# Performance work log

Hardware: AMD Instinct MI355X
Metric: run time of the kernel (lower is better)

Reference implementation:

```python
import jax, jax.numpy as jnp
import numpy as np

B, S, E, H, I = 32, 257, 1024, 16, 4096
D = E // H  # head_dim = 64
EPS = 1e-5


def setup_inputs() -> dict:
    key = jax.random.key(0)
    ks = jax.random.split(key, 12)
    std = 0.02
    inp = {
        'hidden_states': jax.random.normal(ks[0], (B, S, E), jnp.float32),
        'attention_mask': jnp.zeros((B, 1, S, S), jnp.float32),
        'causal_attention_mask': jnp.zeros((B, 1, S, S), jnp.float32),
        'ln1_w': jnp.ones((E,), jnp.float32),
        'ln1_b': jnp.zeros((E,), jnp.float32),
        'q_w': jax.random.normal(ks[1], (E, E), jnp.float32) * std,
        'q_b': jnp.zeros((E,), jnp.float32),
        'k_w': jax.random.normal(ks[2], (E, E), jnp.float32) * std,
        'k_b': jnp.zeros((E,), jnp.float32),
        'v_w': jax.random.normal(ks[3], (E, E), jnp.float32) * std,
        'v_b': jnp.zeros((E,), jnp.float32),
        'o_w': jax.random.normal(ks[4], (E, E), jnp.float32) * std,
        'o_b': jnp.zeros((E,), jnp.float32),
        'ln2_w': jnp.ones((E,), jnp.float32),
        'ln2_b': jnp.zeros((E,), jnp.float32),
        'fc1_w': jax.random.normal(ks[5], (I, E), jnp.float32) * std,
        'fc1_b': jnp.zeros((I,), jnp.float32),
        'fc2_w': jax.random.normal(ks[6], (E, I), jnp.float32) * std,
        'fc2_b': jnp.zeros((E,), jnp.float32),
    }
    return inp


def _layernorm(x, w, b):
    mu = jnp.mean(x, axis=-1, keepdims=True)
    var = jnp.mean(jnp.square(x - mu), axis=-1, keepdims=True)
    return (x - mu) * jax.lax.rsqrt(var + EPS) * w + b


def _gelu_tanh(x):
    # 0.5*x*(1+tanh(sqrt(2/pi)*(x+0.044715*x^3)))
    c = np.sqrt(2.0 / np.pi).astype(np.float32)
    return 0.5 * x * (1.0 + jnp.tanh(c * (x + 0.044715 * x * x * x)))


def reference(hidden_states, attention_mask, causal_attention_mask,
              ln1_w, ln1_b, q_w, q_b, k_w, k_b, v_w, v_b, o_w, o_b,
              ln2_w, ln2_b, fc1_w, fc1_b, fc2_w, fc2_b):
    scale = D ** -0.5
    residual = hidden_states
    x = _layernorm(hidden_states, ln1_w, ln1_b)

    # projections (torch Linear: x @ W.T + b), q pre-scaled as in source
    q = (x @ q_w.T + q_b) * scale
    k = x @ k_w.T + k_b
    v = x @ v_w.T + v_b

    # [B, H, S, D]
    q = q.reshape(B, S, H, D).transpose(0, 2, 1, 3)
    k = k.reshape(B, S, H, D).transpose(0, 2, 1, 3)
    v = v.reshape(B, S, H, D).transpose(0, 2, 1, 3)

    scores = jnp.einsum('bhqd,bhkd->bhqk', q, k)  # [B,H,S,S]
    scores = scores + causal_attention_mask + attention_mask
    probs = jax.nn.softmax(scores, axis=-1)
    ctx = jnp.einsum('bhqk,bhkd->bhqd', probs, v)
    ctx = ctx.transpose(0, 2, 1, 3).reshape(B, S, E)
    attn_out = ctx @ o_w.T + o_b

    h = residual + attn_out
    residual = h
    x = _layernorm(h, ln2_w, ln2_b)
    x = _gelu_tanh(x @ fc1_w.T + fc1_b)
    x = x @ fc2_w.T + fc2_b
    return residual + x
```

## Files before the change

### kernel.cpp

```cpp
#include <hip/hip_runtime.h>

typedef unsigned short u16;
typedef unsigned int   u32;
typedef short s16x8 __attribute__((ext_vector_type(8)));
typedef float f32x4 __attribute__((ext_vector_type(4)));

#define MFMA16(A,B,C) __builtin_amdgcn_mfma_f32_16x16x32_bf16((A),(B),(C),0,0,0)
#define BAR()  asm volatile("s_barrier" ::: "memory")
#define VMC8   asm volatile("s_waitcnt vmcnt(8)" ::: "memory")
#define VMC0   asm volatile("s_waitcnt vmcnt(0)" ::: "memory")

#define B_   32
#define S_   257
#define E_   1024
#define H_   16
#define D_   64
#define I_   4096
#define M_   (B_*S_)

__device__ __forceinline__ u16 f2bf(float f) {
    u32 u = __float_as_uint(f);
    u32 r = u + 0x7fffu + ((u >> 16) & 1u);
    return (u16)(r >> 16);
}
__device__ __forceinline__ float bf2f(u16 b) {
    return __uint_as_float(((u32)b) << 16);
}

__device__ __forceinline__ void gload16(const void* g, void* l) {
    __builtin_amdgcn_global_load_lds(
        (const __attribute__((address_space(1))) u32*)g,
        (__attribute__((address_space(3))) u32*)l, 16, 0, 0);
}

__global__ __launch_bounds__(256)
void convert_w_kernel(const float* __restrict__ qw, const float* __restrict__ kw,
                      const float* __restrict__ vw, const float* __restrict__ ow,
                      const float* __restrict__ f1, const float* __restrict__ f2,
                      u16* __restrict__ dst)
{
    const int total4 = (12 * 1048576) / 4;
    for (int i = blockIdx.x * 256 + threadIdx.x; i < total4; i += gridDim.x * 256) {
        int e = i * 4;
        int seg = e >> 20;
        const float* srcp; int off;
        if (seg < 4)      { srcp = (seg == 0 ? qw : seg == 1 ? kw : seg == 2 ? vw : ow); off = e & 1048575; }
        else if (seg < 8) { srcp = f1; off = e - 4 * 1048576; }
        else              { srcp = f2; off = e - 8 * 1048576; }
        float4 v = *(const float4*)(srcp + off);
        ushort4 o;
        o.x = f2bf(v.x); o.y = f2bf(v.y); o.z = f2bf(v.z); o.w = f2bf(v.w);
        *(ushort4*)(dst + e) = o;
    }
}

__global__ __launch_bounds__(256)
void mask_combine_kernel(const float* __restrict__ am, const float* __restrict__ cm,
                         u16* __restrict__ msum)
{
    const int total = B_ * S_ * 272;
    for (int i = blockIdx.x * 256 + threadIdx.x; i < total; i += gridDim.x * 256) {
        int skv = i % 272;
        int rem = i / 272;
        int sq  = rem % S_;
        int b   = rem / S_;
        float v;
        if (skv < S_) {
            size_t o = ((size_t)b * S_ + sq) * S_ + skv;
            v = am[o] + cm[o];
        } else v = -1e30f;
        msum[i] = f2bf(v);
    }
}

__global__ __launch_bounds__(256)
void ln_kernel(const float* __restrict__ src, const float* __restrict__ gam,
               const float* __restrict__ bet, u16* __restrict__ dst)
{
    int row = blockIdx.x;
    const float4* p = (const float4*)(src + (size_t)row * E_);
    float4 x = p[threadIdx.x];
    float s  = x.x + x.y + x.z + x.w;
    float s2 = x.x * x.x + x.y * x.y + x.z * x.z + x.w * x.w;
#pragma unroll
    for (int xm = 1; xm < 64; xm <<= 1) {
        s  += __shfl_xor(s,  xm, 64);
        s2 += __shfl_xor(s2, xm, 64);
    }
    __shared__ float red[8];
    int wv = threadIdx.x >> 6;
    if ((threadIdx.x & 63) == 0) { red[wv] = s; red[4 + wv] = s2; }
    __syncthreads();
    s  = red[0] + red[1] + red[2] + red[3];
    s2 = red[4] + red[5] + red[6] + red[7];
    float mu  = s * (1.0f / 1024.0f);
    float var = s2 * (1.0f / 1024.0f) - mu * mu;
    float rs  = rsqrtf(var + 1e-5f);
    float4 g  = ((const float4*)gam)[threadIdx.x];
    float4 be = ((const float4*)bet)[threadIdx.x];
    ushort4 o;
    o.x = f2bf((x.x - mu) * rs * g.x + be.x);
    o.y = f2bf((x.y - mu) * rs * g.y + be.y);
    o.z = f2bf((x.z - mu) * rs * g.z + be.z);
    o.w = f2bf((x.w - mu) * rs * g.w + be.w);
    ((ushort4*)dst)[(size_t)row * 256 + threadIdx.x] = o;
}

template<int MODE>
__global__ __launch_bounds__(512, 2)
void gemmK(const u16* __restrict__ A,
           const u16* __restrict__ Bq, const u16* __restrict__ Bk, const u16* __restrict__ Bv,
           const float* __restrict__ biasq, const float* __restrict__ biask, const float* __restrict__ biasvv,
           const float* __restrict__ res, float* __restrict__ outF, float* __restrict__ outF1,
           u16* __restrict__ outBq, u16* __restrict__ outBk, u16* __restrict__ outBv,
           int M, int N, int Ks, int klen)
{
    __shared__ u16 lds[2][4][8192];
    const int tid = threadIdx.x, lane = tid & 63, w = tid >> 6;
    const int lr = lane & 15, lg = lane >> 4;
    const int wm = w >> 2, wn = w & 3;

    const u16* Bm = Bq; const float* bias = biasq; u16* outB = outBq;
    float scl = 1.0f; int nt = blockIdx.x; int k0 = 0; float* outP = outF;
    if (MODE == 0) {
        int mat = nt >> 2; nt &= 3;
        if (mat == 1)      { Bm = Bk; bias = biask; outB = outBk; }
        else if (mat == 2) { Bm = Bv; bias = biasvv; outB = outBv; }
        if (mat == 0) scl = 0.125f;
    } else if (MODE == 3) {
        int kz = nt & 1; nt >>= 1;
        k0 = kz * klen;
        if (kz) outP = outF1;
    }
    const int m0 = blockIdx.y * 256, n0 = nt * 256;
    const int NTt = klen >> 6;
    const int tb  = k0 >> 6;

    const int p    = w * 1024 + lane * 16;
    const int lby  = p ^ (((p >> 7) & 7) << 4);
    const int srow = lby >> 7;
    const int scol = (lby & 127) >> 1;

    auto STAGEH = [&](int buf, int half, const u16* src, int grow0, int rowmax, int t) {
#pragma unroll
        for (int s = 0; s < 2; ++s) {
            int gr = grow0 + s * 64 + srow; if (gr > rowmax) gr = rowmax;
            gload16(src + (size_t)gr * Ks + ((tb + t) << 6) + scol,
                    (char*)&lds[buf][half][0] + s * 8192 + w * 1024);
        }
    };
    auto STAGE4 = [&](int buf, int t) {
        STAGEH(buf, 0, A,  m0,       M - 1, t);
        STAGEH(buf, 1, A,  m0 + 128, M - 1, t);
        STAGEH(buf, 2, Bm, n0,       N - 1, t);
        STAGEH(buf, 3, Bm, n0 + 128, N - 1, t);
    };
    auto LDA = [&](int buf, int mh, int mf, int kh) -> s16x8 {
        const char* b = (const char*)&lds[buf][wm][0];
        int inrow = mh * 64 + mf * 16 + lr;
        return *(const s16x8*)(b + inrow * 128 + ((kh * 64 + lg * 16) ^ ((lr & 7) << 4)));
    };
    auto LDB = [&](int buf, int nh, int nf, int kh) -> s16x8 {
        const char* b = (const char*)&lds[buf][2 + (wn >> 1)][0];
        int inrow = (wn & 1) * 64 + nh * 32 + nf * 16 + lr;
        return *(const s16x8*)(b + inrow * 128 + ((kh * 64 + lg * 16) ^ ((lr & 7) << 4)));
    };

    f32x4 acc[8][4];
#pragma unroll
    for (int i = 0; i < 8; ++i)
#pragma unroll
        for (int j = 0; j < 4; ++j) { f32x4 z = {0.f, 0.f, 0.f, 0.f}; acc[i][j] = z; }

    STAGE4(0, 0);
    STAGE4(1, 1);
    VMC8;
    BAR();

    for (int t = 0; t < NTt; ++t) {
        const int cur = t & 1;
        s16x8 bf[2][2][2];
#pragma unroll
        for (int nh = 0; nh < 2; ++nh)
#pragma unroll
            for (int nf = 0; nf < 2; ++nf)
#pragma unroll
                for (int kh = 0; kh < 2; ++kh)
                    bf[nh][nf][kh] = LDB(cur, nh, nf, kh);
#pragma unroll
        for (int mh = 0; mh < 2; ++mh) {
            s16x8 af[4][2];
#pragma unroll
            for (int mf = 0; mf < 4; ++mf)
#pragma unroll
                for (int kh = 0; kh < 2; ++kh)
                    af[mf][kh] = LDA(cur, mh, mf, kh);
#pragma unroll
            for (int mf = 0; mf < 4; ++mf)
#pragma unroll
                for (int nh = 0; nh < 2; ++nh)
#pragma unroll
                    for (int nf = 0; nf < 2; ++nf)
#pragma unroll
                        for (int kh = 0; kh < 2; ++kh)
                            acc[mh * 4 + mf][nh * 2 + nf] =
                                MFMA16(af[mf][kh], bf[nh][nf][kh], acc[mh * 4 + mf][nh * 2 + nf]);
        }
        BAR();
        if (t + 2 < NTt) STAGE4(cur, t + 2);
        if (t + 1 < NTt) {
            if (t + 2 < NTt) { VMC8; } else { VMC0; }
        }
        BAR();
    }

    float biasv[4];
    if (MODE != 3) {
#pragma unroll
        for (int an = 0; an < 4; ++an)
            biasv[an] = bias[n0 + wn * 64 + (an >> 1) * 32 + (an & 1) * 16 + lr];
    }
#pragma unroll
    for (int am = 0; am < 8; ++am) {
#pragma unroll
        for (int r = 0; r < 4; ++r) {
            int row = m0 + wm * 128 + (am >> 2) * 64 + (am & 3) * 16 + lg * 4 + r;
            if (row >= M) continue;
            if (MODE == 0) {
                int bb = row / S_;
                int ss = row - bb * S_;
#pragma unroll
                for (int an = 0; an < 4; ++an) {
                    int col = n0 + wn * 64 + (an >> 1) * 32 + (an & 1) * 16 + lr;
                    int hh = col >> 6, dd = col & 63;
                    float v = (acc[am][an][r] + biasv[an]) * scl;
                    outB[(((size_t)bb * H_ + hh) * S_ + ss) * D_ + dd] = f2bf(v);
                }
            } else if (MODE == 1) {
                size_t base = (size_t)row * N;
#pragma unroll
                for (int an = 0; an < 4; ++an) {
                    int col = n0 + wn * 64 + (an >> 1) * 32 + (an & 1) * 16 + lr;
                    outF[base + col] = acc[am][an][r] + biasv[an] + res[base + col];
                }
            } else if (MODE == 2) {
                size_t base = (size_t)row * N;
#pragma unroll
                for (int an = 0; an < 4; ++an) {
                    int col = n0 + wn * 64 + (an >> 1) * 32 + (an & 1) * 16 + lr;
                    float x = acc[am][an][r] + biasv[an];
                    float u2 = 1.5957691216057308f * (x + 0.044715f * x * x * x);
                    u2 = fminf(u2, 80.0f);
                    float tt = __expf(u2);
                    outB[base + col] = f2bf(x * tt / (1.0f + tt));
                }
            } else {
                size_t base = (size_t)row * N;
#pragma unroll
                for (int an = 0; an < 4; ++an) {
                    int col = n0 + wn * 64 + (an >> 1) * 32 + (an & 1) * 16 + lr;
                    outP[base + col] = acc[am][an][r];
                }
            }
        }
    }
}

__global__ __launch_bounds__(256)
void splitk_reduce(const float* __restrict__ P0, const float* __restrict__ P1,
                   const float* __restrict__ res, const float* __restrict__ bias,
                   float* __restrict__ out)
{
    const int n4 = (M_ * E_) / 4;
    for (int i = blockIdx.x * 256 + threadIdx.x; i < n4; i += gridDim.x * 256) {
        float4 x0 = ((const float4*)P0)[i];
        float4 x1 = ((const float4*)P1)[i];
        float4 rr = ((const float4*)res)[i];
        float4 bb = ((const float4*)bias)[i & 255];
        float4 o;
        o.x = x0.x + x1.x + rr.x + bb.x;
        o.y = x0.y + x1.y + rr.y + bb.y;
        o.z = x0.z + x1.z + rr.z + bb.z;
        o.w = x0.w + x1.w + rr.w + bb.w;
        ((float4*)out)[i] = o;
    }
}

__global__ __launch_bounds__(256)
void attn_kernel(const u16* __restrict__ qg_, const u16* __restrict__ kg_,
                 const u16* __restrict__ vg_, const u16* __restrict__ msum,
                 u16* __restrict__ ctx)
{
    __shared__ u16 Ks[272 * 72];
    __shared__ u16 Vt[64 * 296];
    __shared__ u16 Ps[4][16 * 32];
    const int bh = blockIdx.x;
    const int b = bh >> 4, hh = bh & 15;
    const u16* kg = kg_ + (size_t)bh * (S_ * D_);
    const u16* vg = vg_ + (size_t)bh * (S_ * D_);
    const u16* qg = qg_ + (size_t)bh * (S_ * D_);
    const int tid = threadIdx.x, lane = tid & 63, wv = tid >> 6;

    for (int c = tid; c < (S_ * D_) / 8; c += 256) {
        int s = c >> 3, d8 = (c & 7) << 3;
        s16x8 val = *(const s16x8*)(kg + s * 64 + d8);
        *(s16x8*)&Ks[s * 72 + d8] = val;
    }
    for (int idx = tid; idx < 15 * 64; idx += 256) {
        int rr = 257 + (idx >> 6), cc = idx & 63;
        Ks[rr * 72 + cc] = 0;
    }
    for (int c = tid; c < (S_ * D_) / 8; c += 256) {
        int s = c >> 3, d8 = (c & 7) << 3;
        s16x8 val = *(const s16x8*)(vg + s * 64 + d8);
#pragma unroll
        for (int j = 0; j < 8; ++j) Vt[(d8 + j) * 296 + s] = (u16)val[j];
    }
    for (int idx = tid; idx < 64 * 39; idx += 256) {
        int dd = idx / 39, cc = 257 + idx % 39;
        Vt[dd * 296 + cc] = 0;
    }
    __syncthreads();

    const int lr = lane & 15, lg = lane >> 4;
    for (int qb = wv; qb < 17; qb += 4) {
        const int q0 = qb * 16;
        int qrow = q0 + lr; if (qrow > S_ - 1) qrow = S_ - 1;
        s16x8 aq0 = *(const s16x8*)(qg + qrow * 64 + lg * 8);
        s16x8 aq1 = *(const s16x8*)(qg + qrow * 64 + 32 + lg * 8);

        f32x4 sc[17];
#pragma unroll
        for (int t = 0; t < 17; ++t) { f32x4 z = {0.f, 0.f, 0.f, 0.f}; sc[t] = z; }
#pragma unroll
        for (int t = 0; t < 17; ++t) {
            s16x8 b0 = *(const s16x8*)&Ks[(t * 16 + lr) * 72 + lg * 8];
            s16x8 b1 = *(const s16x8*)&Ks[(t * 16 + lr) * 72 + 32 + lg * 8];
            sc[t] = MFMA16(aq0, b0, sc[t]);
            sc[t] = MFMA16(aq1, b1, sc[t]);
        }
        float mx[4] = {-3e38f, -3e38f, -3e38f, -3e38f};
#pragma unroll
        for (int r = 0; r < 4; ++r) {
            int sq = q0 + lg * 4 + r; if (sq > S_ - 1) sq = S_ - 1;
            const u16* mrow = msum + ((size_t)b * S_ + sq) * 272;
#pragma unroll
            for (int t = 0; t < 17; ++t) {
                sc[t][r] += bf2f(mrow[t * 16 + lr]);
                mx[r] = fmaxf(mx[r], sc[t][r]);
            }
        }
#pragma unroll
        for (int r = 0; r < 4; ++r) {
#pragma unroll
            for (int xm = 1; xm <= 8; xm <<= 1)
                mx[r] = fmaxf(mx[r], __shfl_xor(mx[r], xm, 64));
        }
        float sum[4] = {0.f, 0.f, 0.f, 0.f};
#pragma unroll
        for (int t = 0; t < 17; ++t)
#pragma unroll
            for (int r = 0; r < 4; ++r) {
                float e = __expf(sc[t][r] - mx[r]);
                sc[t][r] = e; sum[r] += e;
            }
#pragma unroll
        for (int r = 0; r < 4; ++r) {
#pragma unroll
            for (int xm = 1; xm <= 8; xm <<= 1)
                sum[r] += __shfl_xor(sum[r], xm, 64);
        }

        f32x4 ac[4];
#pragma unroll
        for (int nt = 0; nt < 4; ++nt) { f32x4 z = {0.f, 0.f, 0.f, 0.f}; ac[nt] = z; }
        u16* myP = &Ps[wv][0];
#pragma unroll
        for (int kc = 0; kc < 9; ++kc) {
#pragma unroll
            for (int tt = 0; tt < 2; ++tt) {
                const int t = kc * 2 + tt;
#pragma unroll
                for (int r = 0; r < 4; ++r) {
                    float pv = (t < 17) ? sc[(t < 17) ? t : 0][r] : 0.f;
                    myP[(lg * 4 + r) * 32 + tt * 16 + lr] = f2bf(pv);
                }
            }
            s16x8 pa = *(const s16x8*)&myP[lr * 32 + lg * 8];
#pragma unroll
            for (int nt = 0; nt < 4; ++nt) {
                s16x8 bv = *(const s16x8*)&Vt[(nt * 16 + lr) * 296 + kc * 32 + lg * 8];
                ac[nt] = MFMA16(pa, bv, ac[nt]);
            }
        }
#pragma unroll
        for (int r = 0; r < 4; ++r) {
            int sq = q0 + lg * 4 + r;
            if (sq < S_) {
                float rd = 1.0f / sum[r];
                size_t base = (((size_t)b * S_ + sq) * H_ + hh) * D_;
#pragma unroll
                for (int nt = 0; nt < 4; ++nt)
                    ctx[base + nt * 16 + lr] = f2bf(ac[nt][r] * rd);
            }
        }
    }
}

extern "C" void kernel_launch(void* const* d_in, const int* in_sizes, int n_in,
                              void* d_out, int out_size, void* d_ws, size_t ws_size,
                              hipStream_t stream)
{
    const float* hid   = (const float*)d_in[0];
    const float* am    = (const float*)d_in[1];
    const float* cm    = (const float*)d_in[2];
    const float* ln1w  = (const float*)d_in[3];
    const float* ln1b  = (const float*)d_in[4];
    const float* qw    = (const float*)d_in[5];
    const float* qbias = (const float*)d_in[6];
    const float* kw    = (const float*)d_in[7];
    const float* kbias = (const float*)d_in[8];
    const float* vw    = (const float*)d_in[9];
    const float* vbias = (const float*)d_in[10];
    const float* ow    = (const float*)d_in[11];
    const float* obias = (const float*)d_in[12];
    const float* ln2w  = (const float*)d_in[13];
    const float* ln2b  = (const float*)d_in[14];
    const float* f1w   = (const float*)d_in[15];
    const float* f1b   = (const float*)d_in[16];
    const float* f2w   = (const float*)d_in[17];
    const float* f2b   = (const float*)d_in[18];
    float* out = (float*)d_out;

    const size_t ME = (size_t)M_ * E_;
    u16* Wq   = (u16*)d_ws;
    u16* Wk   = Wq + 1048576;
    u16* Wv   = Wk + 1048576;
    u16* Wo   = Wv + 1048576;
    u16* Wf1  = Wo + 1048576;
    u16* Wf2  = Wf1 + 4 * 1048576;
    u16* xln  = Wf2 + 4 * 1048576;
    u16* qb_  = xln + ME;
    u16* kb_  = qb_ + ME;
    u16* vb_  = kb_ + ME;
    u16* ctx  = vb_ + ME;
    float* hbuf = (float*)(ctx + ME);
    u16* msum = (u16*)(hbuf + ME);
    u16* act  = qb_;
    u16* x2   = xln;
    float* P0 = (float*)(msum + (size_t)B_ * S_ * 272);
    float* P1 = P0 + ME;
    const size_t need = (size_t)((char*)(P1 + ME) - (char*)d_ws);
    const bool split = ws_size >= need;

    convert_w_kernel<<<3072, 256, 0, stream>>>(qw, kw, vw, ow, f1w, f2w, Wq);
    mask_combine_kernel<<<8736, 256, 0, stream>>>(am, cm, msum);
    ln_kernel<<<M_, 256, 0, stream>>>(hid, ln1w, ln1b, xln);
    gemmK<0><<<dim3(12, 33), 512, 0, stream>>>(xln, Wq, Wk, Wv, qbias, kbias, vbias,
                                               nullptr, nullptr, nullptr, qb_, kb_, vb_,
                                               M_, 1024, 1024, 1024);
    attn_kernel<<<512, 256, 0, stream>>>(qb_, kb_, vb_, msum, ctx);
    if (split) {
        gemmK<3><<<dim3(8, 33), 512, 0, stream>>>(ctx, Wo, nullptr, nullptr, nullptr, nullptr, nullptr,
                                                  nullptr, P0, P1, nullptr, nullptr, nullptr,
                                                  M_, 1024, 1024, 512);
        splitk_reduce<<<2048, 256, 0, stream>>>(P0, P1, hid, obias, hbuf);
    } else {
        gemmK<1><<<dim3(4, 33), 512, 0, stream>>>(ctx, Wo, nullptr, nullptr, obias, nullptr, nullptr,
                                                  hid, hbuf, nullptr, nullptr, nullptr, nullptr,
                                                  M_, 1024, 1024, 1024);
    }
    ln_kernel<<<M_, 256, 0, stream>>>(hbuf, ln2w, ln2b, x2);
    gemmK<2><<<dim3(16, 33), 512, 0, stream>>>(x2, Wf1, nullptr, nullptr, f1b, nullptr, nullptr,
                                               nullptr, nullptr, nullptr, act, nullptr, nullptr,
                                               M_, 4096, 1024, 1024);
    if (split) {
        gemmK<3><<<dim3(8, 33), 512, 0, stream>>>(act, Wf2, nullptr, nullptr, nullptr, nullptr, nullptr,
                                                  nullptr, P0, P1, nullptr, nullptr, nullptr,
                                                  M_, 1024, 4096, 2048);
        splitk_reduce<<<2048, 256, 0, stream>>>(P0, P1, hbuf, f2b, out);
    } else {
        gemmK<1><<<dim3(4, 33), 512, 0, stream>>>(act, Wf2, nullptr, nullptr, f2b, nullptr, nullptr,
                                                  hbuf, out, nullptr, nullptr, nullptr, nullptr,
                                                  M_, 1024, 4096, 4096);
    }
}
```

Before: 451.8 us.

## Replace split-K out-proj and FC2 GEMMs with 128-row tile kernel fusing residual

Removes the split-K path, which wrote two fp32 partial buffers and then ran a separate reduce kernel for the output projection and FC2. A new gemmH kernel uses 128x256 tiles instead of 256x256, doubling the M-dimension grid to 65 row blocks so the N=1024 GEMMs fill the GPU. It adds bias and residual directly in the epilogue. This avoids the extra partial-sum memory traffic and kernel launches. In exchange, each block reuses its loaded B tile across fewer rows, so B traffic per FLOP rises and arithmetic intensity drops.

```diff
diff --git a/kernel.cpp b/kernel.cpp
--- a/kernel.cpp
+++ b/kernel.cpp
@@ -8,6 +8,7 @@
 #define MFMA16(A,B,C) __builtin_amdgcn_mfma_f32_16x16x32_bf16((A),(B),(C),0,0,0)
 #define BAR()  asm volatile("s_barrier" ::: "memory")
 #define VMC8   asm volatile("s_waitcnt vmcnt(8)" ::: "memory")
+#define VMC6   asm volatile("s_waitcnt vmcnt(6)" ::: "memory")
 #define VMC0   asm volatile("s_waitcnt vmcnt(0)" ::: "memory")
 
 #define B_   32
@@ -111,9 +112,8 @@
 void gemmK(const u16* __restrict__ A,
            const u16* __restrict__ Bq, const u16* __restrict__ Bk, const u16* __restrict__ Bv,
            const float* __restrict__ biasq, const float* __restrict__ biask, const float* __restrict__ biasvv,
-           const float* __restrict__ res, float* __restrict__ outF, float* __restrict__ outF1,
            u16* __restrict__ outBq, u16* __restrict__ outBk, u16* __restrict__ outBv,
-           int M, int N, int Ks, int klen)
+           int M, int N, int K)
 {
     __shared__ u16 lds[2][4][8192];
     const int tid = threadIdx.x, lane = tid & 63, w = tid >> 6;
@@ -121,20 +121,15 @@
     const int wm = w >> 2, wn = w & 3;
 
     const u16* Bm = Bq; const float* bias = biasq; u16* outB = outBq;
-    float scl = 1.0f; int nt = blockIdx.x; int k0 = 0; float* outP = outF;
+    float scl = 1.0f; int nt = blockIdx.x;
     if (MODE == 0) {
         int mat = nt >> 2; nt &= 3;
         if (mat == 1)      { Bm = Bk; bias = biask; outB = outBk; }
         else if (mat == 2) { Bm = Bv; bias = biasvv; outB = outBv; }
         if (mat == 0) scl = 0.125f;
-    } else if (MODE == 3) {
-        int kz = nt & 1; nt >>= 1;
-        k0 = kz * klen;
-        if (kz) outP = outF1;
     }
     const int m0 = blockIdx.y * 256, n0 = nt * 256;
-    const int NTt = klen >> 6;
-    const int tb  = k0 >> 6;
+    const int NTt = K >> 6;
 
     const int p    = w * 1024 + lane * 16;
     const int lby  = p ^ (((p >> 7) & 7) << 4);
@@ -145,7 +140,7 @@
 #pragma unroll
         for (int s = 0; s < 2; ++s) {
             int gr = grow0 + s * 64 + srow; if (gr > rowmax) gr = rowmax;
-            gload16(src + (size_t)gr * Ks + ((tb + t) << 6) + scol,
+            gload16(src + (size_t)gr * K + (t << 6) + scol,
                     (char*)&lds[buf][half][0] + s * 8192 + w * 1024);
         }
     };
@@ -215,11 +210,10 @@
     }
 
     float biasv[4];
-    if (MODE != 3) {
-#pragma unroll
-        for (int an = 0; an < 4; ++an)
-            biasv[an] = bias[n0 + wn * 64 + (an >> 1) * 32 + (an & 1) * 16 + lr];
-    }
+#pragma unroll
+    for (int an = 0; an < 4; ++an)
+        biasv[an] = bias[n0 + wn * 64 + (an >> 1) * 32 + (an & 1) * 16 + lr];
+
 #pragma unroll
     for (int am = 0; am < 8; ++am) {
 #pragma unroll
@@ -236,14 +230,7 @@
                     float v = (acc[am][an][r] + biasv[an]) * scl;
                     outB[(((size_t)bb * H_ + hh) * S_ + ss) * D_ + dd] = f2bf(v);
                 }
-            } else if (MODE == 1) {
-                size_t base = (size_t)row * N;
-#pragma unroll
-                for (int an = 0; an < 4; ++an) {
-                    int col = n0 + wn * 64 + (an >> 1) * 32 + (an & 1) * 16 + lr;
-                    outF[base + col] = acc[am][an][r] + biasv[an] + res[base + col];
-                }
-            } else if (MODE == 2) {
+            } else {
                 size_t base = (size_t)row * N;
 #pragma unroll
                 for (int an = 0; an < 4; ++an) {
@@ -254,35 +241,110 @@
                     float tt = __expf(u2);
                     outB[base + col] = f2bf(x * tt / (1.0f + tt));
                 }
-            } else {
-                size_t base = (size_t)row * N;
-#pragma unroll
-                for (int an = 0; an < 4; ++an) {
-                    int col = n0 + wn * 64 + (an >> 1) * 32 + (an & 1) * 16 + lr;
-                    outP[base + col] = acc[am][an][r];
-                }
-            }
-        }
-    }
-}
-
-__global__ __launch_bounds__(256)
-void splitk_reduce(const float* __restrict__ P0, const float* __restrict__ P1,
-                   const float* __restrict__ res, const float* __restrict__ bias,
-                   float* __restrict__ out)
-{
-    const int n4 = (M_ * E_) / 4;
-    for (int i = blockIdx.x * 256 + threadIdx.x; i < n4; i += gridDim.x * 256) {
-        float4 x0 = ((const float4*)P0)[i];
-        float4 x1 = ((const float4*)P1)[i];
-        float4 rr = ((const float4*)res)[i];
-        float4 bb = ((const float4*)bias)[i & 255];
-        float4 o;
-        o.x = x0.x + x1.x + rr.x + bb.x;
-        o.y = x0.y + x1.y + rr.y + bb.y;
-        o.z = x0.z + x1.z + rr.z + bb.z;
-        o.w = x0.w + x1.w + rr.w + bb.w;
-        ((float4*)out)[i] = o;
+            }
+        }
+    }
+}
+
+__global__ __launch_bounds__(512, 2)
+void gemmH(const u16* __restrict__ A, const u16* __restrict__ Bw,
+           const float* __restrict__ bias, const float* __restrict__ res,
+           float* __restrict__ outF, int M, int N, int K)
+{
+    __shared__ u16 lds[2][3][8192];
+    const int tid = threadIdx.x, lane = tid & 63, w = tid >> 6;
+    const int lr = lane & 15, lg = lane >> 4;
+    const int wm = w >> 2, wn = w & 3;
+
+    const int m0 = blockIdx.y * 128, n0 = blockIdx.x * 256;
+    const int NTt = K >> 6;
+
+    const int p    = w * 1024 + lane * 16;
+    const int lby  = p ^ (((p >> 7) & 7) << 4);
+    const int srow = lby >> 7;
+    const int scol = (lby & 127) >> 1;
+
+    auto STAGEH = [&](int buf, int half, const u16* src, int grow0, int rowmax, int t) {
+#pragma unroll
+        for (int s = 0; s < 2; ++s) {
+            int gr = grow0 + s * 64 + srow; if (gr > rowmax) gr = rowmax;
+            gload16(src + (size_t)gr * K + (t << 6) + scol,
+                    (char*)&lds[buf][half][0] + s * 8192 + w * 1024);
+        }
+    };
+    auto STAGE3 = [&](int buf, int t) {
+        STAGEH(buf, 0, A,  m0,       M - 1, t);
+        STAGEH(buf, 1, Bw, n0,       N - 1, t);
+        STAGEH(buf, 2, Bw, n0 + 128, N - 1, t);
+    };
+    auto LDA = [&](int buf, int mf, int kh) -> s16x8 {
+        const char* b = (const char*)&lds[buf][0][0];
+        int inrow = wm * 64 + mf * 16 + lr;
+        return *(const s16x8*)(b + inrow * 128 + ((kh * 64 + lg * 16) ^ ((lr & 7) << 4)));
+    };
+    auto LDB = [&](int buf, int nf, int kh) -> s16x8 {
+        const char* b = (const char*)&lds[buf][1 + (wn >> 1)][0];
+        int inrow = (wn & 1) * 64 + nf * 16 + lr;
+        return *(const s16x8*)(b + inrow * 128 + ((kh * 64 + lg * 16) ^ ((lr & 7) << 4)));
+    };
+
+    f32x4 acc[4][4];
+#pragma unroll
+    for (int i = 0; i < 4; ++i)
+#pragma unroll
+        for (int j = 0; j < 4; ++j) { f32x4 z = {0.f, 0.f, 0.f, 0.f}; acc[i][j] = z; }
+
+    STAGE3(0, 0);
+    STAGE3(1, 1);
+    VMC6;
+    BAR();
+
+    for (int t = 0; t < NTt; ++t) {
+        const int cur = t & 1;
+        s16x8 bf[4][2], af[4][2];
+#pragma unroll
+        for (int nf = 0; nf < 4; ++nf)
+#pragma unroll
+            for (int kh = 0; kh < 2; ++kh)
+                bf[nf][kh] = LDB(cur, nf, kh);
+#pragma unroll
+        for (int mf = 0; mf < 4; ++mf)
+#pragma unroll
+            for (int kh = 0; kh < 2; ++kh)
+                af[mf][kh] = LDA(cur, mf, kh);
+#pragma unroll
+        for (int mf = 0; mf < 4; ++mf)
+#pragma unroll
+            for (int nf = 0; nf < 4; ++nf)
+#pragma unroll
+                for (int kh = 0; kh < 2; ++kh)
+                    acc[mf][nf] = MFMA16(af[mf][kh], bf[nf][kh], acc[mf][nf]);
+        BAR();
+        if (t + 2 < NTt) STAGE3(cur, t + 2);
+        if (t + 1 < NTt) {
+            if (t + 2 < NTt) { VMC6; } else { VMC0; }
+        }
+        BAR();
+    }
+
+    float biasv[4];
+#pragma unroll
+    for (int nf = 0; nf < 4; ++nf)
+        biasv[nf] = bias[n0 + wn * 64 + nf * 16 + lr];
+
+#pragma unroll
+    for (int mf = 0; mf < 4; ++mf) {
+#pragma unroll
+        for (int r = 0; r < 4; ++r) {
+            int row = m0 + wm * 64 + mf * 16 + lg * 4 + r;
+            if (row >= M) continue;
+            size_t base = (size_t)row * N;
+#pragma unroll
+            for (int nf = 0; nf < 4; ++nf) {
+                int col = n0 + wn * 64 + nf * 16 + lr;
+                outF[base + col] = acc[mf][nf][r] + biasv[nf] + res[base + col];
+            }
+        }
     }
 }
 
@@ -448,40 +510,16 @@
     u16* msum = (u16*)(hbuf + ME);
     u16* act  = qb_;
     u16* x2   = xln;
-    float* P0 = (float*)(msum + (size_t)B_ * S_ * 272);
-    float* P1 = P0 + ME;
-    const size_t need = (size_t)((char*)(P1 + ME) - (char*)d_ws);
-    const bool split = ws_size >= need;
 
     convert_w_kernel<<<3072, 256, 0, stream>>>(qw, kw, vw, ow, f1w, f2w, Wq);
     mask_combine_kernel<<<8736, 256, 0, stream>>>(am, cm, msum);
     ln_kernel<<<M_, 256, 0, stream>>>(hid, ln1w, ln1b, xln);
     gemmK<0><<<dim3(12, 33), 512, 0, stream>>>(xln, Wq, Wk, Wv, qbias, kbias, vbias,
-                                               nullptr, nullptr, nullptr, qb_, kb_, vb_,
-                                               M_, 1024, 1024, 1024);
+                                               qb_, kb_, vb_, M_, 1024, 1024);
     attn_kernel<<<512, 256, 0, stream>>>(qb_, kb_, vb_, msum, ctx);
-    if (split) {
-        gemmK<3><<<dim3(8, 33), 512, 0, stream>>>(ctx, Wo, nullptr, nullptr, nullptr, nullptr, nullptr,
-                                                  nullptr, P0, P1, nullptr, nullptr, nullptr,
-                                                  M_, 1024, 1024, 512);
-        splitk_reduce<<<2048, 256, 0, stream>>>(P0, P1, hid, obias, hbuf);
-    } else {
-        gemmK<1><<<dim3(4, 33), 512, 0, stream>>>(ctx, Wo, nullptr, nullptr, obias, nullptr, nullptr,
-                                                  hid, hbuf, nullptr, nullptr, nullptr, nullptr,
-                                                  M_, 1024, 1024, 1024);
-    }
+    gemmH<<<dim3(4, 65), 512, 0, stream>>>(ctx, Wo, obias, hid, hbuf, M_, 1024, 1024);
     ln_kernel<<<M_, 256, 0, stream>>>(hbuf, ln2w, ln2b, x2);
     gemmK<2><<<dim3(16, 33), 512, 0, stream>>>(x2, Wf1, nullptr, nullptr, f1b, nullptr, nullptr,
-                                               nullptr, nullptr, nullptr, act, nullptr, nullptr,
-                                               M_, 4096, 1024, 1024);
-    if (split) {
-        gemmK<3><<<dim3(8, 33), 512, 0, stream>>>(act, Wf2, nullptr, nullptr, nullptr, nullptr, nullptr,
-                                                  nullptr, P0, P1, nullptr, nullptr, nullptr,
-                                                  M_, 1024, 4096, 2048);
-        splitk_reduce<<<2048, 256, 0, stream>>>(P0, P1, hbuf, f2b, out);
-    } else {
-        gemmK<1><<<dim3(4, 33), 512, 0, stream>>>(act, Wf2, nullptr, nullptr, f2b, nullptr, nullptr,
-                                                  hbuf, out, nullptr, nullptr, nullptr, nullptr,
-                                                  M_, 1024, 4096, 4096);
-    }
-}
+                                               act, nullptr, nullptr, M_, 4096, 1024);
+    gemmH<<<dim3(4, 65), 512, 0, stream>>>(act, Wf2, f2b, hbuf, out, M_, 1024, 4096);
+}
```

Result: faster. 440.8 us (-2.4%).
